# Kernel tuning notes

Hardware: AMD Instinct MI355X
Metric: run time of the kernel (lower is better)

Reference implementation:

```python
import jax, jax.numpy as jnp
import numpy as np

N_NODES = 100000
N_EDGES = 3200000
IN_CH, HID, OUT_CH = 602, 16, 41


def setup_inputs() -> dict:
    key = jax.random.key(0)
    ks = jax.random.split(key, 5)
    x = jax.random.normal(ks[0], (N_NODES, IN_CH), dtype=jnp.float32)
    edge_index = jax.random.randint(ks[1], (2, N_EDGES), 0, N_NODES, dtype=jnp.int32)
    # glorot init for weights, zeros for biases (matches reset_parameters)
    W1 = jax.random.normal(ks[2], (IN_CH, HID), dtype=jnp.float32) * np.sqrt(2.0 / (IN_CH + HID))
    b1 = jnp.zeros((HID,), dtype=jnp.float32)
    W2 = jax.random.normal(ks[3], (HID, OUT_CH), dtype=jnp.float32) * np.sqrt(2.0 / (HID + OUT_CH))
    b2 = jnp.zeros((OUT_CH,), dtype=jnp.float32)
    return {"x": x, "edge_index": edge_index, "W1": W1, "b1": b1, "W2": W2, "b2": b2}


def _sage_conv(x, src, dst, W, b, n_nodes):
    # linear transform first (16-wide), then gather-scatter-mean over edges
    h = x @ W                                   # [N, out]
    msg = h[src]                                # [E, out] gather of source nodes
    agg = jax.ops.segment_sum(msg, dst, num_segments=n_nodes)          # [N, out]
    cnt = jax.ops.segment_sum(jnp.ones((src.shape[0], 1), h.dtype), dst,
                              num_segments=n_nodes)                     # [N, 1]
    mean = agg / jnp.maximum(cnt, 1.0)          # scatter-mean (0 for isolated nodes)
    return mean + b


def reference(x, edge_index, W1, b1, W2, b2):
    src, dst = edge_index[0], edge_index[1]     # source_to_target flow
    n = x.shape[0]
    h = jax.nn.relu(_sage_conv(x, src, dst, W1, b1, n))
    # F.dropout(training=False) -> identity (inference mode)
    out = _sage_conv(h, src, dst, W2, b2, n)
    return jax.nn.log_softmax(out, axis=1)
```

## Files before the change

### kernel.cpp

```cpp
#include <hip/hip_runtime.h>
#include <hip/hip_fp16.h>
#include <cmath>

#define NN 100000
#define NE 3200000
#define CIN 602
#define CH 16
#define COUT 41
#define TB 128
#define KTL 32
#define KSPLIT 4

#define NPB 128
#define NB  ((NN + NPB - 1) / NPB)
#define EPC 32
#define ECHUNK (256 * EPC)
#define EB  ((NE + ECHUNK - 1) / ECHUNK)

__device__ float    g_part[KSPLIT * NN * CH];
__device__ __half   g_h1h[NN * CH];
__device__ __half   g_h1bh[NN * CH];
__device__ int      g_rs[NN + 1];
__device__ int      g_csr[NE];
__device__ unsigned g_pack[NE];
__device__ int      g_cnt[NB * EB];
__device__ int      g_colsum[NB];
__device__ int      g_bbase[NB + 1];

__device__ __forceinline__ int clamp_node(int v) {
    return v < 0 ? 0 : (v >= NN ? NN - 1 : v);
}

__global__ __launch_bounds__(256) void fallback_zero_out_k(float* __restrict__ out, int n) {
    int i = blockIdx.x * blockDim.x + threadIdx.x;
    if (i < n) out[i] = 0.0f;
}

__global__ __launch_bounds__(256) void count_k(const int* __restrict__ ei) {
    __shared__ int h[NB];
    const int t = threadIdx.x;
    for (int i = t; i < NB; i += 256) h[i] = 0;
    __syncthreads();
    const int base = blockIdx.x * ECHUNK;
#pragma unroll
    for (int j = 0; j < EPC; ++j) {
        int e = base + j * 256 + t;
        if (e < NE) {
            int d = clamp_node(ei[NE + e]);
            atomicAdd(&h[d >> 7], 1);
        }
    }
    __syncthreads();
    for (int i = t; i < NB; i += 256) g_cnt[i * EB + blockIdx.x] = h[i];
}

__global__ __launch_bounds__(256) void scanA_k() {
    const int b = blockIdx.x;
    const int t = threadIdx.x;
    __shared__ int a[512];
    __shared__ int sh[256];
    a[t]       = (t < EB)       ? g_cnt[b * EB + t]       : 0;
    a[t + 256] = (t + 256 < EB) ? g_cnt[b * EB + t + 256] : 0;
    __syncthreads();
    int e0 = a[2 * t], e1 = a[2 * t + 1];
    int sum = e0 + e1;
    sh[t] = sum;
    __syncthreads();
    for (int off = 1; off < 256; off <<= 1) {
        int v = (t >= off) ? sh[t - off] : 0;
        __syncthreads();
        sh[t] += v;
        __syncthreads();
    }
    int run = sh[t] - sum;
    if (2 * t < EB)     g_cnt[b * EB + 2 * t]     = run;
    if (2 * t + 1 < EB) g_cnt[b * EB + 2 * t + 1] = run + e0;
    if (t == 255) g_colsum[b] = sh[255];
}

__global__ __launch_bounds__(1024) void scanB_k() {
    const int t = threadIdx.x;
    __shared__ int sh[1024];
    int v = (t < NB) ? g_colsum[t] : 0;
    sh[t] = v;
    __syncthreads();
    for (int off = 1; off < 1024; off <<= 1) {
        int u = (t >= off) ? sh[t - off] : 0;
        __syncthreads();
        sh[t] += u;
        __syncthreads();
    }
    if (t < NB) g_bbase[t] = sh[t] - v;
    if (t == 1023) {
        g_bbase[NB] = sh[1023];
        g_rs[NN]    = sh[1023];
    }
}

__global__ __launch_bounds__(256) void scatter_k(const int* __restrict__ ei) {
    __shared__ int lb[NB];
    const int t = threadIdx.x;
    for (int i = t; i < NB; i += 256)
        lb[i] = g_bbase[i] + g_cnt[i * EB + blockIdx.x];
    __syncthreads();
    const int base = blockIdx.x * ECHUNK;
#pragma unroll
    for (int j = 0; j < EPC; ++j) {
        int e = base + j * 256 + t;
        if (e < NE) {
            int s = clamp_node(ei[e]);
            int d = clamp_node(ei[NE + e]);
            int p = atomicAdd(&lb[d >> 7], 1);
            g_pack[p] = (unsigned)s | ((unsigned)(d & 127) << 17);
        }
    }
}

__global__ __launch_bounds__(256) void build_k() {
    const int b = blockIdx.x;
    const int t = threadIdx.x;
    const int n0 = b * NPB;
    const int e0 = g_bbase[b], e1 = g_bbase[b + 1];
    __shared__ int ldeg[NPB];
    __shared__ int lrs[NPB + 1];
    __shared__ int lcur[NPB];
    if (t < NPB) ldeg[t] = 0;
    __syncthreads();
    for (int e = e0 + t; e < e1; e += 256) {
        unsigned v = g_pack[e];
        atomicAdd(&ldeg[v >> 17], 1);
    }
    __syncthreads();
    if (t == 0) {
        int run = 0;
        for (int i = 0; i < NPB; ++i) { lrs[i] = run; run += ldeg[i]; }
        lrs[NPB] = run;
    }
    __syncthreads();
    if (t < NPB) {
        int node = n0 + t;
        if (node < NN) g_rs[node] = e0 + lrs[t];
        lcur[t] = lrs[t];
    }
    __syncthreads();
    for (int e = e0 + t; e < e1; e += 256) {
        unsigned v = g_pack[e];
        int r = atomicAdd(&lcur[v >> 17], 1);
        g_csr[e0 + r] = (int)(v & 0x1FFFF);
    }
}

__global__ __launch_bounds__(TB) void gemm1_k(const float* __restrict__ x,
                                              const float* __restrict__ W1) {
    __shared__ float xs[KTL][TB + 1];
    const int bid = blockIdx.x;
    const int h   = bid & 3;
    const int rblk = bid >> 2;
    const int t = threadIdx.x;
    const int l  = t & 15;
    const int rg = t >> 4;
    const int row0 = rblk * TB;
    const int row  = row0 + t;
    const int kbase = h * 160;
    const int NT = (h < 3) ? 5 : 4;

    float acc[CH];
#pragma unroll
    for (int c = 0; c < CH; ++c) acc[c] = 0.f;

    float2 ld[16];

    auto stage_load = [&](int ti) {
        const int kb = kbase + KTL * ti;
        const bool colok = (h < 3) || (ti < 3) || (l <= 12);
#pragma unroll
        for (int p = 0; p < 16; ++p) {
            int rgl = row0 + rg + 8 * p;
            ld[p] = (rgl < NN && colok)
                ? *reinterpret_cast<const float2*>(x + (size_t)rgl * CIN + kb + 2 * l)
                : make_float2(0.f, 0.f);
        }
    };
    auto stage_store = [&]() {
#pragma unroll
        for (int p = 0; p < 16; ++p) {
            int rl = rg + 8 * p;
            xs[2 * l][rl]     = ld[p].x;
            xs[2 * l + 1][rl] = ld[p].y;
        }
    };
    auto fma_col = [&](int krow, float xv) {
        const float4* w4 = reinterpret_cast<const float4*>(W1 + (size_t)krow * CH);
        float4 w0 = w4[0], w1 = w4[1], w2 = w4[2], w3 = w4[3];
        acc[0]  += xv * w0.x; acc[1]  += xv * w0.y; acc[2]  += xv * w0.z; acc[3]  += xv * w0.w;
        acc[4]  += xv * w1.x; acc[5]  += xv * w1.y; acc[6]  += xv * w1.z; acc[7]  += xv * w1.w;
        acc[8]  += xv * w2.x; acc[9]  += xv * w2.y; acc[10] += xv * w2.z; acc[11] += xv * w2.w;
        acc[12] += xv * w3.x; acc[13] += xv * w3.y; acc[14] += xv * w3.z; acc[15] += xv * w3.w;
    };

    stage_load(0);
    for (int ti = 0; ti < NT; ++ti) {
        stage_store();
        __syncthreads();
        if (ti < NT - 1) stage_load(ti + 1);
        const int kb = kbase + KTL * ti;
        if (h < 3 || ti < 3) {
#pragma unroll 8
            for (int kk = 0; kk < KTL; ++kk) fma_col(kb + kk, xs[kk][t]);
        } else {
#pragma unroll 13
            for (int kk = 0; kk < 26; ++kk) fma_col(kb + kk, xs[kk][t]);
        }
        __syncthreads();
    }

    if (row < NN) {
        float4* pp = reinterpret_cast<float4*>(g_part + ((size_t)h * NN + row) * CH);
        pp[0] = make_float4(acc[0],  acc[1],  acc[2],  acc[3]);
        pp[1] = make_float4(acc[4],  acc[5],  acc[6],  acc[7]);
        pp[2] = make_float4(acc[8],  acc[9],  acc[10], acc[11]);
        pp[3] = make_float4(acc[12], acc[13], acc[14], acc[15]);
    }
}

__global__ __launch_bounds__(256) void combine_k() {
    int node = blockIdx.x * blockDim.x + threadIdx.x;
    if (node >= NN) return;
    float s[CH];
#pragma unroll
    for (int h = 0; h < KSPLIT; ++h) {
        const float4* pp = reinterpret_cast<const float4*>(g_part + ((size_t)h * NN + node) * CH);
        float4 p0 = pp[0], p1 = pp[1], p2 = pp[2], p3 = pp[3];
        if (h == 0) {
            s[0]=p0.x; s[1]=p0.y; s[2]=p0.z; s[3]=p0.w;
            s[4]=p1.x; s[5]=p1.y; s[6]=p1.z; s[7]=p1.w;
            s[8]=p2.x; s[9]=p2.y; s[10]=p2.z; s[11]=p2.w;
            s[12]=p3.x; s[13]=p3.y; s[14]=p3.z; s[15]=p3.w;
        } else {
            s[0]+=p0.x; s[1]+=p0.y; s[2]+=p0.z; s[3]+=p0.w;
            s[4]+=p1.x; s[5]+=p1.y; s[6]+=p1.z; s[7]+=p1.w;
            s[8]+=p2.x; s[9]+=p2.y; s[10]+=p2.z; s[11]+=p2.w;
            s[12]+=p3.x; s[13]+=p3.y; s[14]+=p3.z; s[15]+=p3.w;
        }
    }
    __half2 pk[8];
#pragma unroll
    for (int c = 0; c < 8; ++c)
        pk[c] = __float22half2_rn(make_float2(s[2 * c], s[2 * c + 1]));
    uint4* hp = reinterpret_cast<uint4*>(&g_h1h[(size_t)node * CH]);
    hp[0] = *reinterpret_cast<uint4*>(&pk[0]);
    hp[1] = *reinterpret_cast<uint4*>(&pk[4]);
}

__global__ __launch_bounds__(256) void gather1_k(const float* __restrict__ b1) {
    int gtid = blockIdx.x * blockDim.x + threadIdx.x;
    int node = gtid >> 6;
    int l    = gtid & 63;
    int q    = l & 3;
    int es   = l >> 2;
    int start = g_rs[node], end = g_rs[node + 1];
    float4 acc = make_float4(0.f, 0.f, 0.f, 0.f);
    int e = start + es;
    for (; e + 16 < end; e += 32) {
        int s0 = g_csr[e], s1 = g_csr[e + 16];
        uint2 ua = *reinterpret_cast<const uint2*>(&g_h1h[(size_t)s0 * CH + (q << 2)]);
        uint2 ub = *reinterpret_cast<const uint2*>(&g_h1h[(size_t)s1 * CH + (q << 2)]);
        float2 fa0 = __half22float2(*reinterpret_cast<__half2*>(&ua.x));
        float2 fa1 = __half22float2(*reinterpret_cast<__half2*>(&ua.y));
        float2 fb0 = __half22float2(*reinterpret_cast<__half2*>(&ub.x));
        float2 fb1 = __half22float2(*reinterpret_cast<__half2*>(&ub.y));
        acc.x += fa0.x + fb0.x; acc.y += fa0.y + fb0.y;
        acc.z += fa1.x + fb1.x; acc.w += fa1.y + fb1.y;
    }
    if (e < end) {
        int s0 = g_csr[e];
        uint2 ua = *reinterpret_cast<const uint2*>(&g_h1h[(size_t)s0 * CH + (q << 2)]);
        float2 fa0 = __half22float2(*reinterpret_cast<__half2*>(&ua.x));
        float2 fa1 = __half22float2(*reinterpret_cast<__half2*>(&ua.y));
        acc.x += fa0.x; acc.y += fa0.y; acc.z += fa1.x; acc.w += fa1.y;
    }
#pragma unroll
    for (int off = 4; off < 64; off <<= 1) {
        acc.x += __shfl_xor(acc.x, off, 64);
        acc.y += __shfl_xor(acc.y, off, 64);
        acc.z += __shfl_xor(acc.z, off, 64);
        acc.w += __shfl_xor(acc.w, off, 64);
    }
    if (l < 4) {
        float inv = 1.0f / fmaxf((float)(end - start), 1.0f);
        float4 bv = reinterpret_cast<const float4*>(b1)[l];
        __half2 h0 = __float22half2_rn(make_float2(fmaxf(acc.x * inv + bv.x, 0.f),
                                                   fmaxf(acc.y * inv + bv.y, 0.f)));
        __half2 h1 = __float22half2_rn(make_float2(fmaxf(acc.z * inv + bv.z, 0.f),
                                                   fmaxf(acc.w * inv + bv.w, 0.f)));
        uint2 u;
        u.x = *reinterpret_cast<unsigned*>(&h0);
        u.y = *reinterpret_cast<unsigned*>(&h1);
        *reinterpret_cast<uint2*>(&g_h1bh[(size_t)node * CH + (l << 2)]) = u;
    }
}

__global__ __launch_bounds__(256) void g2final_k(const float* __restrict__ W2,
                                                 const float* __restrict__ b2,
                                                 float* __restrict__ out) {
    __shared__ float w2s[CH * COUT];
    const int t = threadIdx.x;
    for (int i = t; i < CH * COUT; i += 256) w2s[i] = W2[i];
    __syncthreads();

    int gtid = blockIdx.x * blockDim.x + t;
    int node = gtid >> 6;
    int l    = gtid & 63;
    int q    = l & 3;
    int es   = l >> 2;
    int start = g_rs[node], end = g_rs[node + 1];
    float4 acc = make_float4(0.f, 0.f, 0.f, 0.f);
    int e = start + es;
    for (; e + 16 < end; e += 32) {
        int s0 = g_csr[e], s1 = g_csr[e + 16];
        uint2 ua = *reinterpret_cast<const uint2*>(&g_h1bh[(size_t)s0 * CH + (q << 2)]);
        uint2 ub = *reinterpret_cast<const uint2*>(&g_h1bh[(size_t)s1 * CH + (q << 2)]);
        float2 fa0 = __half22float2(*reinterpret_cast<__half2*>(&ua.x));
        float2 fa1 = __half22float2(*reinterpret_cast<__half2*>(&ua.y));
        float2 fb0 = __half22float2(*reinterpret_cast<__half2*>(&ub.x));
        float2 fb1 = __half22float2(*reinterpret_cast<__half2*>(&ub.y));
        acc.x += fa0.x + fb0.x; acc.y += fa0.y + fb0.y;
        acc.z += fa1.x + fb1.x; acc.w += fa1.y + fb1.y;
    }
    if (e < end) {
        int s0 = g_csr[e];
        uint2 ua = *reinterpret_cast<const uint2*>(&g_h1bh[(size_t)s0 * CH + (q << 2)]);
        float2 fa0 = __half22float2(*reinterpret_cast<__half2*>(&ua.x));
        float2 fa1 = __half22float2(*reinterpret_cast<__half2*>(&ua.y));
        acc.x += fa0.x; acc.y += fa0.y; acc.z += fa1.x; acc.w += fa1.y;
    }
#pragma unroll
    for (int off = 4; off < 64; off <<= 1) {
        acc.x += __shfl_xor(acc.x, off, 64);
        acc.y += __shfl_xor(acc.y, off, 64);
        acc.z += __shfl_xor(acc.z, off, 64);
        acc.w += __shfl_xor(acc.w, off, 64);
    }
    float a16[CH];
#pragma unroll
    for (int k = 0; k < CH; ++k) {
        float comp = ((k & 3) == 0) ? acc.x : ((k & 3) == 1) ? acc.y
                   : ((k & 3) == 2) ? acc.z : acc.w;
        a16[k] = __shfl(comp, k >> 2, 64);
    }
    float inv = 1.0f / fmaxf((float)(end - start), 1.0f);
    float o = -INFINITY;
    if (l < COUT) {
        float s = 0.f;
#pragma unroll
        for (int k = 0; k < CH; ++k) s += a16[k] * w2s[k * COUT + l];
        o = s * inv + b2[l];
    }
    float m = o;
#pragma unroll
    for (int off = 32; off > 0; off >>= 1) m = fmaxf(m, __shfl_xor(m, off, 64));
    float ex = (l < COUT) ? expf(o - m) : 0.0f;
    float ssum = ex;
#pragma unroll
    for (int off = 32; off > 0; off >>= 1) ssum += __shfl_xor(ssum, off, 64);
    if (l < COUT)
        __builtin_nontemporal_store(o - m - logf(ssum), &out[(size_t)node * COUT + l]);
}

extern "C" void kernel_launch(void* const* d_in, const int* in_sizes, int n_in,
                              void* d_out, int out_size, void* d_ws, size_t ws_size,
                              hipStream_t stream) {
    (void)d_ws; (void)ws_size;
    float* out = (float*)d_out;

    const int expect[6] = {NN * CIN, 2 * NE, CIN * CH, CH, CH * COUT, COUT};
    bool ok = (n_in >= 6) && (out_size == NN * COUT);
    if (ok) {
        for (int i = 0; i < 6; ++i)
            if (in_sizes[i] != expect[i]) { ok = false; break; }
    }
    if (!ok) {
        int n = out_size > 0 ? out_size : 1;
        fallback_zero_out_k<<<(n + 255) / 256, 256, 0, stream>>>(out, n);
        return;
    }

    const float* x  = (const float*)d_in[0];
    const int*   ei = (const int*)d_in[1];
    const float* W1 = (const float*)d_in[2];
    const float* b1 = (const float*)d_in[3];
    const float* W2 = (const float*)d_in[4];
    const float* b2 = (const float*)d_in[5];

    const int WAVE_BLKS = (NN * 64 + 255) / 256;
    const int G1_BLKS   = ((NN + TB - 1) / TB) * KSPLIT;

    count_k  <<<EB, 256, 0, stream>>>(ei);
    scanA_k  <<<NB, 256, 0, stream>>>();
    scanB_k  <<<1, 1024, 0, stream>>>();
    scatter_k<<<EB, 256, 0, stream>>>(ei);
    build_k  <<<NB, 256, 0, stream>>>();
    gemm1_k  <<<G1_BLKS, TB, 0, stream>>>(x, W1);
    combine_k<<<(NN + 255) / 256, 256, 0, stream>>>();
    gather1_k<<<WAVE_BLKS, 256, 0, stream>>>(b1);
    g2final_k<<<WAVE_BLKS, 256, 0, stream>>>(W2, b2, out);
}
```

Baseline: 593.0 us.

## Replace per-node CSR gather with bucketed shared-memory atomic aggregation

Removes the build_k pass that turned destination buckets into a full CSR. Both aggregation kernels now process each 128-node bucket of packed edges in one block and accumulate features into shared memory with rotated-index atomics; degrees are counted in the first pass and stored as inverse degrees. The second layer computes the 16x41 projection and log-softmax per node in one thread and stages the output through shared memory for coalesced stores. This saves a pass over the edges and the CSR memory traffic, at the cost of shared-memory atomic contention and fewer, heavier blocks with a large per-thread register array.

```diff
diff --git a/kernel.cpp b/kernel.cpp
--- a/kernel.cpp
+++ b/kernel.cpp
@@ -20,8 +20,7 @@
 __device__ float    g_part[KSPLIT * NN * CH];
 __device__ __half   g_h1h[NN * CH];
 __device__ __half   g_h1bh[NN * CH];
-__device__ int      g_rs[NN + 1];
-__device__ int      g_csr[NE];
+__device__ float    g_invd[NN];
 __device__ unsigned g_pack[NE];
 __device__ int      g_cnt[NB * EB];
 __device__ int      g_colsum[NB];
@@ -91,10 +90,7 @@
         __syncthreads();
     }
     if (t < NB) g_bbase[t] = sh[t] - v;
-    if (t == 1023) {
-        g_bbase[NB] = sh[1023];
-        g_rs[NN]    = sh[1023];
-    }
+    if (t == 1023) g_bbase[NB] = sh[1023];
 }
 
 __global__ __launch_bounds__(256) void scatter_k(const int* __restrict__ ei) {
@@ -113,40 +109,6 @@
             int p = atomicAdd(&lb[d >> 7], 1);
             g_pack[p] = (unsigned)s | ((unsigned)(d & 127) << 17);
         }
-    }
-}
-
-__global__ __launch_bounds__(256) void build_k() {
-    const int b = blockIdx.x;
-    const int t = threadIdx.x;
-    const int n0 = b * NPB;
-    const int e0 = g_bbase[b], e1 = g_bbase[b + 1];
-    __shared__ int ldeg[NPB];
-    __shared__ int lrs[NPB + 1];
-    __shared__ int lcur[NPB];
-    if (t < NPB) ldeg[t] = 0;
-    __syncthreads();
-    for (int e = e0 + t; e < e1; e += 256) {
-        unsigned v = g_pack[e];
-        atomicAdd(&ldeg[v >> 17], 1);
-    }
-    __syncthreads();
-    if (t == 0) {
-        int run = 0;
-        for (int i = 0; i < NPB; ++i) { lrs[i] = run; run += ldeg[i]; }
-        lrs[NPB] = run;
-    }
-    __syncthreads();
-    if (t < NPB) {
-        int node = n0 + t;
-        if (node < NN) g_rs[node] = e0 + lrs[t];
-        lcur[t] = lrs[t];
-    }
-    __syncthreads();
-    for (int e = e0 + t; e < e1; e += 256) {
-        unsigned v = g_pack[e];
-        int r = atomicAdd(&lcur[v >> 17], 1);
-        g_csr[e0 + r] = (int)(v & 0x1FFFF);
     }
 }
 
@@ -252,119 +214,126 @@
     hp[1] = *reinterpret_cast<uint4*>(&pk[4]);
 }
 
-__global__ __launch_bounds__(256) void gather1_k(const float* __restrict__ b1) {
-    int gtid = blockIdx.x * blockDim.x + threadIdx.x;
-    int node = gtid >> 6;
-    int l    = gtid & 63;
-    int q    = l & 3;
-    int es   = l >> 2;
-    int start = g_rs[node], end = g_rs[node + 1];
-    float4 acc = make_float4(0.f, 0.f, 0.f, 0.f);
-    int e = start + es;
-    for (; e + 16 < end; e += 32) {
-        int s0 = g_csr[e], s1 = g_csr[e + 16];
-        uint2 ua = *reinterpret_cast<const uint2*>(&g_h1h[(size_t)s0 * CH + (q << 2)]);
-        uint2 ub = *reinterpret_cast<const uint2*>(&g_h1h[(size_t)s1 * CH + (q << 2)]);
-        float2 fa0 = __half22float2(*reinterpret_cast<__half2*>(&ua.x));
-        float2 fa1 = __half22float2(*reinterpret_cast<__half2*>(&ua.y));
-        float2 fb0 = __half22float2(*reinterpret_cast<__half2*>(&ub.x));
-        float2 fb1 = __half22float2(*reinterpret_cast<__half2*>(&ub.y));
-        acc.x += fa0.x + fb0.x; acc.y += fa0.y + fb0.y;
-        acc.z += fa1.x + fb1.x; acc.w += fa1.y + fb1.y;
-    }
-    if (e < end) {
-        int s0 = g_csr[e];
-        uint2 ua = *reinterpret_cast<const uint2*>(&g_h1h[(size_t)s0 * CH + (q << 2)]);
-        float2 fa0 = __half22float2(*reinterpret_cast<__half2*>(&ua.x));
-        float2 fa1 = __half22float2(*reinterpret_cast<__half2*>(&ua.y));
-        acc.x += fa0.x; acc.y += fa0.y; acc.z += fa1.x; acc.w += fa1.y;
-    }
-#pragma unroll
-    for (int off = 4; off < 64; off <<= 1) {
-        acc.x += __shfl_xor(acc.x, off, 64);
-        acc.y += __shfl_xor(acc.y, off, 64);
-        acc.z += __shfl_xor(acc.z, off, 64);
-        acc.w += __shfl_xor(acc.w, off, 64);
-    }
-    if (l < 4) {
-        float inv = 1.0f / fmaxf((float)(end - start), 1.0f);
-        float4 bv = reinterpret_cast<const float4*>(b1)[l];
-        __half2 h0 = __float22half2_rn(make_float2(fmaxf(acc.x * inv + bv.x, 0.f),
-                                                   fmaxf(acc.y * inv + bv.y, 0.f)));
-        __half2 h1 = __float22half2_rn(make_float2(fmaxf(acc.z * inv + bv.z, 0.f),
-                                                   fmaxf(acc.w * inv + bv.w, 0.f)));
-        uint2 u;
-        u.x = *reinterpret_cast<unsigned*>(&h0);
-        u.y = *reinterpret_cast<unsigned*>(&h1);
-        *reinterpret_cast<uint2*>(&g_h1bh[(size_t)node * CH + (l << 2)]) = u;
-    }
-}
-
-__global__ __launch_bounds__(256) void g2final_k(const float* __restrict__ W2,
-                                                 const float* __restrict__ b2,
-                                                 float* __restrict__ out) {
+__global__ __launch_bounds__(256) void bgather1_k(const float* __restrict__ b1) {
+    __shared__ float acc[NPB * CH];
+    __shared__ int   ldeg[NPB];
+    const int b = blockIdx.x;
+    const int t = threadIdx.x;
+    for (int i = t; i < NPB * CH; i += 256) acc[i] = 0.f;
+    if (t < NPB) ldeg[t] = 0;
+    __syncthreads();
+    const int e0 = g_bbase[b], e1 = g_bbase[b + 1];
+    for (int e = e0 + t; e < e1; e += 256) {
+        unsigned v = g_pack[e];
+        int src = (int)(v & 0x1FFFF);
+        int ld  = (int)(v >> 17);
+        const uint4* rp = reinterpret_cast<const uint4*>(&g_h1h[(size_t)src * CH]);
+        uint4 r0 = rp[0], r1 = rp[1];
+        atomicAdd(&ldeg[ld], 1);
+        float* ab = acc + ld * CH;
+#pragma unroll
+        for (int i = 0; i < 4; ++i) {
+            unsigned w = (i == 0) ? r0.x : (i == 1) ? r0.y : (i == 2) ? r0.z : r0.w;
+            float2 f = __half22float2(*reinterpret_cast<const __half2*>(&w));
+            atomicAdd(&ab[((2 * i)     + ld) & 15], f.x);
+            atomicAdd(&ab[((2 * i + 1) + ld) & 15], f.y);
+        }
+#pragma unroll
+        for (int i = 0; i < 4; ++i) {
+            unsigned w = (i == 0) ? r1.x : (i == 1) ? r1.y : (i == 2) ? r1.z : r1.w;
+            float2 f = __half22float2(*reinterpret_cast<const __half2*>(&w));
+            atomicAdd(&ab[((2 * i + 8) + ld) & 15], f.x);
+            atomicAdd(&ab[((2 * i + 9) + ld) & 15], f.y);
+        }
+    }
+    __syncthreads();
+    if (t < NPB) {
+        int node = b * NPB + t;
+        if (node < NN) {
+            float inv = 1.0f / fmaxf((float)ldeg[t], 1.0f);
+            g_invd[node] = inv;
+            __half2 pk[8];
+#pragma unroll
+            for (int i = 0; i < 8; ++i) {
+                float lo = acc[t * CH + ((2 * i     + t) & 15)] * inv + b1[2 * i];
+                float hi = acc[t * CH + ((2 * i + 1 + t) & 15)] * inv + b1[2 * i + 1];
+                pk[i] = __float22half2_rn(make_float2(fmaxf(lo, 0.f), fmaxf(hi, 0.f)));
+            }
+            uint4* hp = reinterpret_cast<uint4*>(&g_h1bh[(size_t)node * CH]);
+            hp[0] = *reinterpret_cast<uint4*>(&pk[0]);
+            hp[1] = *reinterpret_cast<uint4*>(&pk[4]);
+        }
+    }
+}
+
+__global__ __launch_bounds__(256) void bg2final_k(const float* __restrict__ W2,
+                                                  const float* __restrict__ b2,
+                                                  float* __restrict__ out) {
+    __shared__ float acc[NPB * CH];
     __shared__ float w2s[CH * COUT];
-    const int t = threadIdx.x;
+    __shared__ float outs[NPB * COUT];
+    const int b = blockIdx.x;
+    const int t = threadIdx.x;
+    for (int i = t; i < NPB * CH; i += 256) acc[i] = 0.f;
     for (int i = t; i < CH * COUT; i += 256) w2s[i] = W2[i];
     __syncthreads();
-
-    int gtid = blockIdx.x * blockDim.x + t;
-    int node = gtid >> 6;
-    int l    = gtid & 63;
-    int q    = l & 3;
-    int es   = l >> 2;
-    int start = g_rs[node], end = g_rs[node + 1];
-    float4 acc = make_float4(0.f, 0.f, 0.f, 0.f);
-    int e = start + es;
-    for (; e + 16 < end; e += 32) {
-        int s0 = g_csr[e], s1 = g_csr[e + 16];
-        uint2 ua = *reinterpret_cast<const uint2*>(&g_h1bh[(size_t)s0 * CH + (q << 2)]);
-        uint2 ub = *reinterpret_cast<const uint2*>(&g_h1bh[(size_t)s1 * CH + (q << 2)]);
-        float2 fa0 = __half22float2(*reinterpret_cast<__half2*>(&ua.x));
-        float2 fa1 = __half22float2(*reinterpret_cast<__half2*>(&ua.y));
-        float2 fb0 = __half22float2(*reinterpret_cast<__half2*>(&ub.x));
-        float2 fb1 = __half22float2(*reinterpret_cast<__half2*>(&ub.y));
-        acc.x += fa0.x + fb0.x; acc.y += fa0.y + fb0.y;
-        acc.z += fa1.x + fb1.x; acc.w += fa1.y + fb1.y;
-    }
-    if (e < end) {
-        int s0 = g_csr[e];
-        uint2 ua = *reinterpret_cast<const uint2*>(&g_h1bh[(size_t)s0 * CH + (q << 2)]);
-        float2 fa0 = __half22float2(*reinterpret_cast<__half2*>(&ua.x));
-        float2 fa1 = __half22float2(*reinterpret_cast<__half2*>(&ua.y));
-        acc.x += fa0.x; acc.y += fa0.y; acc.z += fa1.x; acc.w += fa1.y;
-    }
-#pragma unroll
-    for (int off = 4; off < 64; off <<= 1) {
-        acc.x += __shfl_xor(acc.x, off, 64);
-        acc.y += __shfl_xor(acc.y, off, 64);
-        acc.z += __shfl_xor(acc.z, off, 64);
-        acc.w += __shfl_xor(acc.w, off, 64);
-    }
-    float a16[CH];
-#pragma unroll
-    for (int k = 0; k < CH; ++k) {
-        float comp = ((k & 3) == 0) ? acc.x : ((k & 3) == 1) ? acc.y
-                   : ((k & 3) == 2) ? acc.z : acc.w;
-        a16[k] = __shfl(comp, k >> 2, 64);
-    }
-    float inv = 1.0f / fmaxf((float)(end - start), 1.0f);
-    float o = -INFINITY;
-    if (l < COUT) {
-        float s = 0.f;
-#pragma unroll
-        for (int k = 0; k < CH; ++k) s += a16[k] * w2s[k * COUT + l];
-        o = s * inv + b2[l];
-    }
-    float m = o;
-#pragma unroll
-    for (int off = 32; off > 0; off >>= 1) m = fmaxf(m, __shfl_xor(m, off, 64));
-    float ex = (l < COUT) ? expf(o - m) : 0.0f;
-    float ssum = ex;
-#pragma unroll
-    for (int off = 32; off > 0; off >>= 1) ssum += __shfl_xor(ssum, off, 64);
-    if (l < COUT)
-        __builtin_nontemporal_store(o - m - logf(ssum), &out[(size_t)node * COUT + l]);
+    const int e0 = g_bbase[b], e1 = g_bbase[b + 1];
+    for (int e = e0 + t; e < e1; e += 256) {
+        unsigned v = g_pack[e];
+        int src = (int)(v & 0x1FFFF);
+        int ld  = (int)(v >> 17);
+        const uint4* rp = reinterpret_cast<const uint4*>(&g_h1bh[(size_t)src * CH]);
+        uint4 r0 = rp[0], r1 = rp[1];
+        float* ab = acc + ld * CH;
+#pragma unroll
+        for (int i = 0; i < 4; ++i) {
+            unsigned w = (i == 0) ? r0.x : (i == 1) ? r0.y : (i == 2) ? r0.z : r0.w;
+            float2 f = __half22float2(*reinterpret_cast<const __half2*>(&w));
+            atomicAdd(&ab[((2 * i)     + ld) & 15], f.x);
+            atomicAdd(&ab[((2 * i + 1) + ld) & 15], f.y);
+        }
+#pragma unroll
+        for (int i = 0; i < 4; ++i) {
+            unsigned w = (i == 0) ? r1.x : (i == 1) ? r1.y : (i == 2) ? r1.z : r1.w;
+            float2 f = __half22float2(*reinterpret_cast<const __half2*>(&w));
+            atomicAdd(&ab[((2 * i + 8) + ld) & 15], f.x);
+            atomicAdd(&ab[((2 * i + 9) + ld) & 15], f.y);
+        }
+    }
+    __syncthreads();
+    if (t < NPB) {
+        int node = b * NPB + t;
+        if (node < NN) {
+            float inv = g_invd[node];
+            float a16[CH];
+#pragma unroll
+            for (int c = 0; c < CH; ++c) a16[c] = acc[t * CH + ((c + t) & 15)];
+            float o[COUT];
+#pragma unroll
+            for (int j = 0; j < COUT; ++j) o[j] = 0.f;
+#pragma unroll
+            for (int k = 0; k < CH; ++k) {
+                float a = a16[k];
+#pragma unroll
+                for (int j = 0; j < COUT; ++j) o[j] += a * w2s[k * COUT + j];
+            }
+            float m = -INFINITY;
+#pragma unroll
+            for (int j = 0; j < COUT; ++j) { o[j] = o[j] * inv + b2[j]; m = fmaxf(m, o[j]); }
+            float ssum = 0.f;
+#pragma unroll
+            for (int j = 0; j < COUT; ++j) ssum += expf(o[j] - m);
+            float lg = m + logf(ssum);
+#pragma unroll
+            for (int j = 0; j < COUT; ++j) outs[t * COUT + j] = o[j] - lg;
+        }
+    }
+    __syncthreads();
+    int lim = NN - b * NPB; if (lim > NPB) lim = NPB;
+    lim *= COUT;
+    float* ob = out + (size_t)b * NPB * COUT;
+    for (int i = t; i < lim; i += 256)
+        __builtin_nontemporal_store(outs[i], &ob[i]);
 }
 
 extern "C" void kernel_launch(void* const* d_in, const int* in_sizes, int n_in,
@@ -392,16 +361,14 @@
     const float* W2 = (const float*)d_in[4];
     const float* b2 = (const float*)d_in[5];
 
-    const int WAVE_BLKS = (NN * 64 + 255) / 256;
-    const int G1_BLKS   = ((NN + TB - 1) / TB) * KSPLIT;
-
-    count_k  <<<EB, 256, 0, stream>>>(ei);
-    scanA_k  <<<NB, 256, 0, stream>>>();
-    scanB_k  <<<1, 1024, 0, stream>>>();
-    scatter_k<<<EB, 256, 0, stream>>>(ei);
-    build_k  <<<NB, 256, 0, stream>>>();
-    gemm1_k  <<<G1_BLKS, TB, 0, stream>>>(x, W1);
-    combine_k<<<(NN + 255) / 256, 256, 0, stream>>>();
-    gather1_k<<<WAVE_BLKS, 256, 0, stream>>>(b1);
-    g2final_k<<<WAVE_BLKS, 256, 0, stream>>>(W2, b2, out);
-}
+    const int G1_BLKS = ((NN + TB - 1) / TB) * KSPLIT;
+
+    count_k   <<<EB, 256, 0, stream>>>(ei);
+    scanA_k   <<<NB, 256, 0, stream>>>();
+    scanB_k   <<<1, 1024, 0, stream>>>();
+    scatter_k <<<EB, 256, 0, stream>>>(ei);
+    gemm1_k   <<<G1_BLKS, TB, 0, stream>>>(x, W1);
+    combine_k <<<(NN + 255) / 256, 256, 0, stream>>>();
+    bgather1_k<<<NB, 256, 0, stream>>>(b1);
+    bg2final_k<<<NB, 256, 0, stream>>>(W2, b2, out);
+}
```

After: 1.134 ms. +91.2%, slower.
